# Kernel tuning notes

Hardware: AMD Instinct MI355X
Metric: run time of the kernel (lower is better)

Reference implementation:

```python
import jax, jax.numpy as jnp
import numpy as np

N_NODES = 100000
N_EDGES = 1600000
D_IN = 128
D_EMB = 128


def setup_inputs() -> dict:
    key = jax.random.key(0)
    ks = jax.random.split(key, 8)
    x = jax.random.normal(ks[0], (N_NODES, D_IN), dtype=jnp.float32)
    src = jax.random.randint(ks[1], (N_EDGES,), 0, N_NODES, dtype=jnp.int32)
    dst = jax.random.randint(ks[2], (N_EDGES,), 0, N_NODES, dtype=jnp.int32)
    # Glorot-ish init for GraphConv weights
    s = 1.0 / np.sqrt(D_EMB)
    W0 = jax.random.normal(ks[3], (D_IN, D_EMB), dtype=jnp.float32) * s
    W1 = jax.random.normal(ks[4], (D_EMB, D_EMB), dtype=jnp.float32) * s
    W2 = jax.random.normal(ks[5], (D_EMB, D_EMB), dtype=jnp.float32) * s
    b0 = jnp.zeros((D_EMB,), jnp.float32)
    b1 = jnp.zeros((D_EMB,), jnp.float32)
    b2 = jnp.zeros((D_EMB,), jnp.float32)
    return {"x": x, "src": src, "dst": dst,
            "W0": W0, "b0": b0, "W1": W1, "b1": b1, "W2": W2, "b2": b2}


def _graph_conv(h, src, dst, norm_src, norm_dst, W, b):
    # DGL GraphConv, norm='both': D_out^{-1/2} A D_in^{-1/2} H W + b
    h = h * norm_src[:, None]                       # scale src features
    m = jax.ops.segment_sum(h[src], dst, num_segments=N_NODES)  # SpMM aggregate
    m = m * norm_dst[:, None]
    return m @ W + b


def reference(x, src, dst, W0, b0, W1, b1, W2, b2):
    ones = jnp.ones((N_EDGES,), jnp.float32)
    out_deg = jax.ops.segment_sum(ones, src, num_segments=N_NODES)
    in_deg = jax.ops.segment_sum(ones, dst, num_segments=N_NODES)
    norm_src = jax.lax.rsqrt(jnp.clip(out_deg, 1.0))
    norm_dst = jax.lax.rsqrt(jnp.clip(in_deg, 1.0))

    h = x
    Ws = (W0, W1, W2)
    bs = (b0, b1, b2)
    n_layers = len(Ws)
    for layer in range(n_layers):
        h = _graph_conv(h, src, dst, norm_src, norm_dst, Ws[layer], bs[layer])
        if layer != n_layers - 1:
            h = jax.nn.relu(h)  # dropout is identity in eval mode
    return h
```

## Files before the change

kernel.cpp:

```cpp
#include <hip/hip_runtime.h>
#include <hip/hip_bf16.h>

#define N_NODES 100000
#define N_EDGES 1600000
#define D 128
#define NB 1563
#define PB 256
#define CHUNK 6250
#define SCANL (NB * PB)
#define ECAP 2560

typedef __attribute__((ext_vector_type(8))) short bf16x8;
typedef __attribute__((ext_vector_type(4))) float f32x4;

__device__ __forceinline__ float bf2f(unsigned short u) {
    unsigned int x = ((unsigned int)u) << 16;
    return __builtin_bit_cast(float, x);
}
__device__ __forceinline__ unsigned short f2bf(float f) {
    unsigned int x = __builtin_bit_cast(unsigned int, f);
    x += 0x7fffu + ((x >> 16) & 1u);
    return (unsigned short)(x >> 16);
}

__global__ __launch_bounds__(1024) void k_pcount(const int* __restrict__ src, const int* __restrict__ dst,
                                                 int* __restrict__ cntD, int* __restrict__ cntS) {
    __shared__ int hd[NB];
    __shared__ int hs[NB];
    int t = threadIdx.x, blk = blockIdx.x;
    for (int i = t; i < NB; i += 1024) { hd[i] = 0; hs[i] = 0; }
    __syncthreads();
    int base = blk * CHUNK;
    for (int i = t; i < CHUNK; i += 1024) {
        int e = base + i;
        if (e < N_EDGES) {
            atomicAdd(&hd[dst[e] >> 6], 1);
            atomicAdd(&hs[src[e] >> 6], 1);
        }
    }
    __syncthreads();
    for (int i = t; i < NB; i += 1024) {
        cntD[i * PB + blk] = hd[i];
        cntS[i * PB + blk] = hs[i];
    }
}

__global__ void k_scan1(int* __restrict__ a, int* __restrict__ bs, int n) {
    __shared__ int tmp[256];
    int t = threadIdx.x;
    int i = blockIdx.x * 256 + t;
    int v = (i < n) ? a[i] : 0;
    tmp[t] = v; __syncthreads();
    for (int off = 1; off < 256; off <<= 1) {
        int x = (t >= off) ? tmp[t - off] : 0;
        __syncthreads();
        tmp[t] += x;
        __syncthreads();
    }
    if (i < n) a[i] = tmp[t] - v;
    if (t == 255) bs[blockIdx.x] = tmp[255];
}

__global__ void k_scan2(int* __restrict__ bs, int nb) {
    __shared__ int tmp[1024];
    int t = threadIdx.x;
    int i0 = 2 * t, i1 = 2 * t + 1;
    int a = (i0 < nb) ? bs[i0] : 0;
    int b = (i1 < nb) ? bs[i1] : 0;
    int s = a + b;
    tmp[t] = s; __syncthreads();
    for (int off = 1; off < 1024; off <<= 1) {
        int x = (t >= off) ? tmp[t - off] : 0;
        __syncthreads();
        tmp[t] += x;
        __syncthreads();
    }
    int excl = tmp[t] - s;
    if (i0 < nb) bs[i0] = excl;
    if (i1 < nb) bs[i1] = excl + a;
}

__global__ void k_scan3(int* __restrict__ a, const int* __restrict__ bs, int n) {
    int i = blockIdx.x * 256 + threadIdx.x;
    if (i < n) a[i] += bs[blockIdx.x];
}

__global__ __launch_bounds__(1024) void k_pscatter(const int* __restrict__ src, const int* __restrict__ dst,
                                                   const int* __restrict__ scanD, const int* __restrict__ scanS,
                                                   unsigned int* __restrict__ pairD, unsigned char* __restrict__ srcS) {
    __shared__ int od[NB];
    __shared__ int osx[NB];
    int t = threadIdx.x, blk = blockIdx.x;
    for (int i = t; i < NB; i += 1024) {
        od[i] = scanD[i * PB + blk];
        osx[i] = scanS[i * PB + blk];
    }
    __syncthreads();
    int base = blk * CHUNK;
    for (int i = t; i < CHUNK; i += 1024) {
        int e = base + i;
        if (e < N_EDGES) {
            int s = src[e], d = dst[e];
            int pd = atomicAdd(&od[d >> 6], 1);
            pairD[pd] = ((unsigned int)(d & 63) << 26) | (unsigned int)s;
            int ps = atomicAdd(&osx[s >> 6], 1);
            srcS[ps] = (unsigned char)(s & 63);
        }
    }
}

__global__ __launch_bounds__(256) void k_normsrc(const unsigned char* __restrict__ srcS,
                                                 const int* __restrict__ scanS, float* __restrict__ ns) {
    __shared__ int c[64];
    int b = blockIdx.x, t = threadIdx.x;
    if (t < 64) c[t] = 0;
    __syncthreads();
    int beg = scanS[b * PB];
    int end = (b < NB - 1) ? scanS[(b + 1) * PB] : N_EDGES;
    for (int i = beg + t; i < end; i += 256) atomicAdd(&c[srcS[i]], 1);
    __syncthreads();
    if (t < 64) {
        int g = b * 64 + t;
        if (g < N_NODES) {
            int a = c[t]; if (a < 1) a = 1;
            ns[g] = rsqrtf((float)a);
        }
    }
}

__global__ __launch_bounds__(256) void k_bsort(const unsigned int* __restrict__ pairD,
                                               const int* __restrict__ scanD,
                                               int* __restrict__ esrc,
                                               int* __restrict__ rowbeg,
                                               int* __restrict__ degD) {
    __shared__ int cnt[64], off[64], cur[64];
    int b = blockIdx.x, t = threadIdx.x;
    int lane = t & 63, wave = t >> 6;
    if (t < 64) cnt[t] = 0;
    __syncthreads();
    int beg = scanD[b * PB];
    int end = (b < NB - 1) ? scanD[(b + 1) * PB] : N_EDGES;
    int n = end - beg;
    for (int i = t; i < n; i += 256) atomicAdd(&cnt[pairD[beg + i] >> 26], 1);
    __syncthreads();
    if (wave == 0) {
        int v = cnt[lane];
        int x = v;
        for (int o = 1; o < 64; o <<= 1) { int y = __shfl_up(x, o); if (lane >= o) x += y; }
        off[lane] = x - v;
        cur[lane] = x - v;
    }
    __syncthreads();
    if (t < 64) {
        int g = b * 64 + t;
        if (g < N_NODES) { rowbeg[g] = beg + off[t]; degD[g] = cnt[t]; }
    }
    for (int i = t; i < n; i += 256) {
        unsigned int p = pairD[beg + i];
        int pos = atomicAdd(&cur[p >> 26], 1);
        esrc[beg + pos] = (int)(p & 0x3FFFFFFu);
    }
}

__global__ void k_cvt(const float* __restrict__ x, const float* __restrict__ ns,
                      unsigned short* __restrict__ xb, int n4) {
    int i = blockIdx.x * 256 + threadIdx.x;
    if (i < n4) {
        int row = i >> 5;
        float sc = ns[row];
        const float4 v = ((const float4*)x)[i];
        unsigned int lo = (unsigned int)f2bf(v.x * sc) | ((unsigned int)f2bf(v.y * sc) << 16);
        unsigned int hi = (unsigned int)f2bf(v.z * sc) | ((unsigned int)f2bf(v.w * sc) << 16);
        ((uint2*)xb)[i] = make_uint2(lo, hi);
    }
}

__global__ void k_transw3(const float* __restrict__ W0, const float* __restrict__ W1,
                          const float* __restrict__ W2, unsigned short* __restrict__ Wt) {
    int gid = blockIdx.x * 256 + threadIdx.x;
    if (gid >= 3 * 2048) return;
    int layer = gid >> 11;
    int di8   = gid & 2047;
    const float* W = (layer == 0) ? W0 : ((layer == 1) ? W1 : W2);
    int di   = di8 * 8;
    int lane = di8 & 63;
    int nt   = (di8 >> 6) & 7;
    int kc   = di8 >> 9;
    int quad = lane >> 4, col = lane & 15;
    unsigned short v[8];
#pragma unroll
    for (int j = 0; j < 8; j++) {
        int k = kc * 32 + quad * 8 + j;
        int nn = nt * 16 + col;
        v[j] = f2bf(W[k * 128 + nn]);
    }
    unsigned short* dp = Wt + (size_t)layer * 16384 + di;
#pragma unroll
    for (int j = 0; j < 8; j++) dp[j] = v[j];
}

__device__ __forceinline__ int aswz(int row, int byte16) {
    return row * 256 + (byte16 ^ ((row & 7) << 4));
}

__global__ __launch_bounds__(512) void k_fused(const unsigned short* __restrict__ hin,
        const int* __restrict__ esrc, const int* __restrict__ rowbeg, const int* __restrict__ degD,
        const int* __restrict__ scanD,
        const unsigned short* __restrict__ Wt, const float* __restrict__ bias,
        const float* __restrict__ nsp, unsigned short* __restrict__ Cb, float* __restrict__ Cf, int M) {
    __shared__ int elist[ECAP];
    __shared__ int rb[64], dg[64];
    __shared__ unsigned short lA[64 * 128];
    int b = blockIdx.x, t = threadIdx.x;
    int lane = t & 63, wave = t >> 6;
    int sub = lane >> 4, col = lane & 15;

    int beg = scanD[b * PB];
    int end = (b < NB - 1) ? scanD[(b + 1) * PB] : N_EDGES;
    int cnt = end - beg;
    if (cnt > ECAP) cnt = ECAP;

    if (t < 64) {
        int g = b * 64 + t;
        rb[t] = (g < M) ? rowbeg[g] : beg;
        dg[t] = (g < M) ? degD[g] : 0;
    }
    for (int i = t; i < cnt; i += 512) elist[i] = esrc[beg + i];
    __syncthreads();

    for (int r = wave; r < 64; r += 8) {
        int ro = rb[r] - beg;
        int dgr = dg[r];
        int re = ro + dgr;
        if (re > ECAP) re = ECAP;
        float acc[8];
#pragma unroll
        for (int j = 0; j < 8; j++) acc[j] = 0.f;
        for (int e = ro; e < re; e += 16) {
            int i0 = e + sub, i1 = e + 4 + sub, i2 = e + 8 + sub, i3 = e + 12 + sub;
            bool v0 = i0 < re, v1 = i1 < re, v2 = i2 < re, v3 = i3 < re;
            int s0 = elist[v0 ? i0 : ro];
            int s1 = elist[v1 ? i1 : ro];
            int s2 = elist[v2 ? i2 : ro];
            int s3 = elist[v3 ? i3 : ro];
            uint4 x0 = *(const uint4*)(hin + (size_t)s0 * D + col * 8);
            uint4 x1 = *(const uint4*)(hin + (size_t)s1 * D + col * 8);
            uint4 x2 = *(const uint4*)(hin + (size_t)s2 * D + col * 8);
            uint4 x3 = *(const uint4*)(hin + (size_t)s3 * D + col * 8);
            if (v0) {
                acc[0] += bf2f((unsigned short)x0.x); acc[1] += bf2f((unsigned short)(x0.x >> 16));
                acc[2] += bf2f((unsigned short)x0.y); acc[3] += bf2f((unsigned short)(x0.y >> 16));
                acc[4] += bf2f((unsigned short)x0.z); acc[5] += bf2f((unsigned short)(x0.z >> 16));
                acc[6] += bf2f((unsigned short)x0.w); acc[7] += bf2f((unsigned short)(x0.w >> 16));
            }
            if (v1) {
                acc[0] += bf2f((unsigned short)x1.x); acc[1] += bf2f((unsigned short)(x1.x >> 16));
                acc[2] += bf2f((unsigned short)x1.y); acc[3] += bf2f((unsigned short)(x1.y >> 16));
                acc[4] += bf2f((unsigned short)x1.z); acc[5] += bf2f((unsigned short)(x1.z >> 16));
                acc[6] += bf2f((unsigned short)x1.w); acc[7] += bf2f((unsigned short)(x1.w >> 16));
            }
            if (v2) {
                acc[0] += bf2f((unsigned short)x2.x); acc[1] += bf2f((unsigned short)(x2.x >> 16));
                acc[2] += bf2f((unsigned short)x2.y); acc[3] += bf2f((unsigned short)(x2.y >> 16));
                acc[4] += bf2f((unsigned short)x2.z); acc[5] += bf2f((unsigned short)(x2.z >> 16));
                acc[6] += bf2f((unsigned short)x2.w); acc[7] += bf2f((unsigned short)(x2.w >> 16));
            }
            if (v3) {
                acc[0] += bf2f((unsigned short)x3.x); acc[1] += bf2f((unsigned short)(x3.x >> 16));
                acc[2] += bf2f((unsigned short)x3.y); acc[3] += bf2f((unsigned short)(x3.y >> 16));
                acc[4] += bf2f((unsigned short)x3.z); acc[5] += bf2f((unsigned short)(x3.z >> 16));
                acc[6] += bf2f((unsigned short)x3.w); acc[7] += bf2f((unsigned short)(x3.w >> 16));
            }
        }
#pragma unroll
        for (int j = 0; j < 8; j++) {
            acc[j] += __shfl_xor(acc[j], 16);
            acc[j] += __shfl_xor(acc[j], 32);
        }
        if (sub == 0) {
            int d2 = dgr; if (d2 < 1) d2 = 1;
            float s = rsqrtf((float)d2);
            uint4 o;
            o.x = (unsigned int)f2bf(acc[0] * s) | ((unsigned int)f2bf(acc[1] * s) << 16);
            o.y = (unsigned int)f2bf(acc[2] * s) | ((unsigned int)f2bf(acc[3] * s) << 16);
            o.z = (unsigned int)f2bf(acc[4] * s) | ((unsigned int)f2bf(acc[5] * s) << 16);
            o.w = (unsigned int)f2bf(acc[6] * s) | ((unsigned int)f2bf(acc[7] * s) << 16);
            *(uint4*)((char*)lA + aswz(r, col * 16)) = o;
        }
    }
    __syncthreads();

    int rt = wave & 3;
    int nh = wave >> 2;
    f32x4 acc2[4];
#pragma unroll
    for (int i = 0; i < 4; i++) acc2[i] = (f32x4){0.f, 0.f, 0.f, 0.f};
    int lr = rt * 16 + col;
#pragma unroll
    for (int kc = 0; kc < 4; kc++) {
        bf16x8 af = *(const bf16x8*)((const char*)lA + aswz(lr, kc * 64 + sub * 16));
#pragma unroll
        for (int j = 0; j < 4; j++) {
            int nt = nh * 4 + j;
            bf16x8 bfr = *(const bf16x8*)(Wt + ((size_t)(kc * 8 + nt) * 64 + lane) * 8);
            acc2[j] = __builtin_amdgcn_mfma_f32_16x16x32_bf16(af, bfr, acc2[j], 0, 0, 0);
        }
    }
    int row0 = b * 64 + rt * 16;
#pragma unroll
    for (int j = 0; j < 4; j++) {
        int nt = nh * 4 + j;
        float bv = bias[nt * 16 + col];
#pragma unroll
        for (int r = 0; r < 4; r++) {
            int rr = row0 + sub * 4 + r;
            if (rr < M) {
                float v = acc2[j][r] + bv;
                if (Cf) {
                    Cf[(size_t)rr * D + nt * 16 + col] = v;
                } else {
                    v = fmaxf(v, 0.f) * nsp[rr];
                    Cb[(size_t)rr * D + nt * 16 + col] = f2bf(v);
                }
            }
        }
    }
}

extern "C" void kernel_launch(void* const* d_in, const int* in_sizes, int n_in,
                              void* d_out, int out_size, void* d_ws, size_t ws_size,
                              hipStream_t stream) {
    const float* x  = (const float*)d_in[0];
    const int* src = (const int*)d_in[1];
    const int* dst = (const int*)d_in[2];
    const float* Wl[3] = {(const float*)d_in[3], (const float*)d_in[5], (const float*)d_in[7]};
    const float* Bl[3] = {(const float*)d_in[4], (const float*)d_in[6], (const float*)d_in[8]};

    const int N = N_NODES, E = N_EDGES;
    const int Mpad = ((N + 63) / 64) * 64;

    char* ws = (char*)d_ws;
    size_t o = 0;
    auto take = [&](size_t bytes) -> void* {
        o = (o + 255) & ~(size_t)255;
        void* p = ws + o;
        o += bytes;
        return p;
    };
    int*   cntD     = (int*)take((size_t)SCANL * 4);
    int*   cntS     = (int*)take((size_t)SCANL * 4);
    int*   bsD      = (int*)take(2048 * 4);
    int*   bsS      = (int*)take(2048 * 4);
    float* norm_src = (float*)take((size_t)N * 4);
    unsigned int*  pairD = (unsigned int*)take((size_t)E * 4);
    unsigned char* srcS  = (unsigned char*)take((size_t)E);
    int*   esrc     = (int*)take((size_t)E * 4);
    int*   rowbeg   = (int*)take((size_t)N * 4);
    int*   degD     = (int*)take((size_t)N * 4);
    unsigned short* Wt   = (unsigned short*)take((size_t)3 * 128 * 128 * 2);
    unsigned short* hA   = (unsigned short*)take((size_t)Mpad * D * 2);
    unsigned short* hB   = (unsigned short*)take((size_t)Mpad * D * 2);

    const int sgrid = SCANL / 256;

    k_pcount<<<PB, 1024, 0, stream>>>(src, dst, cntD, cntS);
    k_scan1<<<sgrid, 256, 0, stream>>>(cntD, bsD, SCANL);
    k_scan2<<<1, 1024, 0, stream>>>(bsD, sgrid);
    k_scan3<<<sgrid, 256, 0, stream>>>(cntD, bsD, SCANL);
    k_scan1<<<sgrid, 256, 0, stream>>>(cntS, bsS, SCANL);
    k_scan2<<<1, 1024, 0, stream>>>(bsS, sgrid);
    k_scan3<<<sgrid, 256, 0, stream>>>(cntS, bsS, SCANL);
    k_pscatter<<<PB, 1024, 0, stream>>>(src, dst, cntD, cntS, pairD, srcS);
    k_normsrc<<<NB, 256, 0, stream>>>(srcS, cntS, norm_src);
    k_bsort<<<NB, 256, 0, stream>>>(pairD, cntD, esrc, rowbeg, degD);

    k_cvt<<<(N * 32 + 255) / 256, 256, 0, stream>>>(x, norm_src, hA, N * 32);
    k_transw3<<<24, 256, 0, stream>>>(Wl[0], Wl[1], Wl[2], Wt);

    k_fused<<<NB, 512, 0, stream>>>(hA, esrc, rowbeg, degD, cntD, Wt,           Bl[0], norm_src, hB, nullptr, N);
    k_fused<<<NB, 512, 0, stream>>>(hB, esrc, rowbeg, degD, cntD, Wt + 16384,   Bl[1], norm_src, hA, nullptr, N);
    k_fused<<<NB, 512, 0, stream>>>(hA, esrc, rowbeg, degD, cntD, Wt + 32768,   Bl[2], nullptr,  nullptr, (float*)d_out, N);
}
```

Before: 417.5 us.

## Replace two-level bucket sort with atomic CSR build and padded sentinel rows

Replaces the partitioned count/scan/scatter/bucket-sort pipeline with a direct global-atomic degree count, a single scan over per-node degrees rounded up to multiples of 16, and an atomic scatter into a CSR whose padding slots hold a sentinel index that points at a zeroed row. The aggregation loop can then drop its per-edge validity checks and the LDS edge staging and read esrc directly. The fused kernel also moves to 256 threads with an occupancy hint, and the source norm is recomputed from degrees instead of stored. The trade-offs are global atomic contention in the scatter, roughly doubled edge storage from padding, wasted gathers on padded slots, and edge order within a row that is no longer deterministic.

```diff
diff --git a/kernel.cpp b/kernel.cpp
--- a/kernel.cpp
+++ b/kernel.cpp
@@ -5,10 +5,8 @@
 #define N_EDGES 1600000
 #define D 128
 #define NB 1563
-#define PB 256
-#define CHUNK 6250
-#define SCANL (NB * PB)
-#define ECAP 2560
+#define SENT N_NODES
+#define ECAP_PAD 3200000
 
 typedef __attribute__((ext_vector_type(8))) short bf16x8;
 typedef __attribute__((ext_vector_type(4))) float f32x4;
@@ -23,33 +21,37 @@
     return (unsigned short)(x >> 16);
 }
 
-__global__ __launch_bounds__(1024) void k_pcount(const int* __restrict__ src, const int* __restrict__ dst,
-                                                 int* __restrict__ cntD, int* __restrict__ cntS) {
-    __shared__ int hd[NB];
-    __shared__ int hs[NB];
-    int t = threadIdx.x, blk = blockIdx.x;
-    for (int i = t; i < NB; i += 1024) { hd[i] = 0; hs[i] = 0; }
-    __syncthreads();
-    int base = blk * CHUNK;
-    for (int i = t; i < CHUNK; i += 1024) {
-        int e = base + i;
-        if (e < N_EDGES) {
-            atomicAdd(&hd[dst[e] >> 6], 1);
-            atomicAdd(&hs[src[e] >> 6], 1);
-        }
-    }
-    __syncthreads();
-    for (int i = t; i < NB; i += 1024) {
-        cntD[i * PB + blk] = hd[i];
-        cntS[i * PB + blk] = hs[i];
-    }
-}
-
-__global__ void k_scan1(int* __restrict__ a, int* __restrict__ bs, int n) {
+__global__ __launch_bounds__(256) void k_zero(int* __restrict__ esrc, int* __restrict__ degS,
+                                              int* __restrict__ degD, int* __restrict__ cur,
+                                              unsigned short* __restrict__ hA, unsigned short* __restrict__ hB) {
+    int i = blockIdx.x * 256 + threadIdx.x;
+    if (i < ECAP_PAD / 4) {
+        ((int4*)esrc)[i] = make_int4(SENT, SENT, SENT, SENT);
+    }
+    if (i < N_NODES) { degS[i] = 0; degD[i] = 0; cur[i] = 0; }
+    if (i < 512) {
+        uint4 z = {0u, 0u, 0u, 0u};
+        ((uint4*)(hA + (size_t)N_NODES * D))[i] = z;
+        ((uint4*)(hB + (size_t)N_NODES * D))[i] = z;
+    }
+}
+
+__global__ __launch_bounds__(256) void k_deg(const int* __restrict__ src, const int* __restrict__ dst,
+                                             int* __restrict__ degS, int* __restrict__ degD) {
+    int e = blockIdx.x * 256 + threadIdx.x;
+    if (e < N_EDGES) {
+        atomicAdd(&degS[src[e]], 1);
+        atomicAdd(&degD[dst[e]], 1);
+    }
+}
+
+__global__ void k_scanA(const int* __restrict__ degD, int* __restrict__ rowbeg,
+                        int* __restrict__ bs, int n) {
     __shared__ int tmp[256];
     int t = threadIdx.x;
     int i = blockIdx.x * 256 + t;
-    int v = (i < n) ? a[i] : 0;
+    int v = 0;
+    if (i < n - 1) v = (degD[i] + 15) & ~15;
     tmp[t] = v; __syncthreads();
     for (int off = 1; off < 256; off <<= 1) {
         int x = (t >= off) ? tmp[t - off] : 0;
@@ -57,7 +59,7 @@
         tmp[t] += x;
         __syncthreads();
     }
-    if (i < n) a[i] = tmp[t] - v;
+    if (i < n) rowbeg[i] = tmp[t] - v;
     if (t == 255) bs[blockIdx.x] = tmp[255];
 }
 
@@ -85,89 +87,24 @@
     if (i < n) a[i] += bs[blockIdx.x];
 }
 
-__global__ __launch_bounds__(1024) void k_pscatter(const int* __restrict__ src, const int* __restrict__ dst,
-                                                   const int* __restrict__ scanD, const int* __restrict__ scanS,
-                                                   unsigned int* __restrict__ pairD, unsigned char* __restrict__ srcS) {
-    __shared__ int od[NB];
-    __shared__ int osx[NB];
-    int t = threadIdx.x, blk = blockIdx.x;
-    for (int i = t; i < NB; i += 1024) {
-        od[i] = scanD[i * PB + blk];
-        osx[i] = scanS[i * PB + blk];
-    }
-    __syncthreads();
-    int base = blk * CHUNK;
-    for (int i = t; i < CHUNK; i += 1024) {
-        int e = base + i;
-        if (e < N_EDGES) {
-            int s = src[e], d = dst[e];
-            int pd = atomicAdd(&od[d >> 6], 1);
-            pairD[pd] = ((unsigned int)(d & 63) << 26) | (unsigned int)s;
-            int ps = atomicAdd(&osx[s >> 6], 1);
-            srcS[ps] = (unsigned char)(s & 63);
-        }
-    }
-}
-
-__global__ __launch_bounds__(256) void k_normsrc(const unsigned char* __restrict__ srcS,
-                                                 const int* __restrict__ scanS, float* __restrict__ ns) {
-    __shared__ int c[64];
-    int b = blockIdx.x, t = threadIdx.x;
-    if (t < 64) c[t] = 0;
-    __syncthreads();
-    int beg = scanS[b * PB];
-    int end = (b < NB - 1) ? scanS[(b + 1) * PB] : N_EDGES;
-    for (int i = beg + t; i < end; i += 256) atomicAdd(&c[srcS[i]], 1);
-    __syncthreads();
-    if (t < 64) {
-        int g = b * 64 + t;
-        if (g < N_NODES) {
-            int a = c[t]; if (a < 1) a = 1;
-            ns[g] = rsqrtf((float)a);
-        }
-    }
-}
-
-__global__ __launch_bounds__(256) void k_bsort(const unsigned int* __restrict__ pairD,
-                                               const int* __restrict__ scanD,
-                                               int* __restrict__ esrc,
-                                               int* __restrict__ rowbeg,
-                                               int* __restrict__ degD) {
-    __shared__ int cnt[64], off[64], cur[64];
-    int b = blockIdx.x, t = threadIdx.x;
-    int lane = t & 63, wave = t >> 6;
-    if (t < 64) cnt[t] = 0;
-    __syncthreads();
-    int beg = scanD[b * PB];
-    int end = (b < NB - 1) ? scanD[(b + 1) * PB] : N_EDGES;
-    int n = end - beg;
-    for (int i = t; i < n; i += 256) atomicAdd(&cnt[pairD[beg + i] >> 26], 1);
-    __syncthreads();
-    if (wave == 0) {
-        int v = cnt[lane];
-        int x = v;
-        for (int o = 1; o < 64; o <<= 1) { int y = __shfl_up(x, o); if (lane >= o) x += y; }
-        off[lane] = x - v;
-        cur[lane] = x - v;
-    }
-    __syncthreads();
-    if (t < 64) {
-        int g = b * 64 + t;
-        if (g < N_NODES) { rowbeg[g] = beg + off[t]; degD[g] = cnt[t]; }
-    }
-    for (int i = t; i < n; i += 256) {
-        unsigned int p = pairD[beg + i];
-        int pos = atomicAdd(&cur[p >> 26], 1);
-        esrc[beg + pos] = (int)(p & 0x3FFFFFFu);
-    }
-}
-
-__global__ void k_cvt(const float* __restrict__ x, const float* __restrict__ ns,
+__global__ __launch_bounds__(256) void k_scatter(const int* __restrict__ src, const int* __restrict__ dst,
+                                                 const int* __restrict__ rowbeg, int* __restrict__ cur,
+                                                 int* __restrict__ esrc) {
+    int e = blockIdx.x * 256 + threadIdx.x;
+    if (e < N_EDGES) {
+        int d = dst[e];
+        int pos = atomicAdd(&cur[d], 1);
+        esrc[rowbeg[d] + pos] = src[e];
+    }
+}
+
+__global__ void k_cvt(const float* __restrict__ x, const int* __restrict__ degS,
                       unsigned short* __restrict__ xb, int n4) {
     int i = blockIdx.x * 256 + threadIdx.x;
     if (i < n4) {
         int row = i >> 5;
-        float sc = ns[row];
+        int dg = degS[row]; if (dg < 1) dg = 1;
+        float sc = rsqrtf((float)dg);
         const float4 v = ((const float4*)x)[i];
         unsigned int lo = (unsigned int)f2bf(v.x * sc) | ((unsigned int)f2bf(v.y * sc) << 16);
         unsigned int hi = (unsigned int)f2bf(v.z * sc) | ((unsigned int)f2bf(v.w * sc) << 16);
@@ -203,74 +140,60 @@
     return row * 256 + (byte16 ^ ((row & 7) << 4));
 }
 
-__global__ __launch_bounds__(512) void k_fused(const unsigned short* __restrict__ hin,
+__global__ __launch_bounds__(256, 8) void k_fused(const unsigned short* __restrict__ hin,
         const int* __restrict__ esrc, const int* __restrict__ rowbeg, const int* __restrict__ degD,
-        const int* __restrict__ scanD,
+        const int* __restrict__ degS,
         const unsigned short* __restrict__ Wt, const float* __restrict__ bias,
-        const float* __restrict__ nsp, unsigned short* __restrict__ Cb, float* __restrict__ Cf, int M) {
-    __shared__ int elist[ECAP];
-    __shared__ int rb[64], dg[64];
+        unsigned short* __restrict__ Cb, float* __restrict__ Cf, int M) {
+    __shared__ int rb[65];
+    __shared__ int dgt[64];
     __shared__ unsigned short lA[64 * 128];
     int b = blockIdx.x, t = threadIdx.x;
     int lane = t & 63, wave = t >> 6;
     int sub = lane >> 4, col = lane & 15;
 
-    int beg = scanD[b * PB];
-    int end = (b < NB - 1) ? scanD[(b + 1) * PB] : N_EDGES;
-    int cnt = end - beg;
-    if (cnt > ECAP) cnt = ECAP;
-
-    if (t < 64) {
+    if (t < 65) {
         int g = b * 64 + t;
-        rb[t] = (g < M) ? rowbeg[g] : beg;
-        dg[t] = (g < M) ? degD[g] : 0;
-    }
-    for (int i = t; i < cnt; i += 512) elist[i] = esrc[beg + i];
+        if (g > N_NODES) g = N_NODES;
+        rb[t] = rowbeg[g];
+        if (t < 64) {
+            int g2 = b * 64 + t;
+            dgt[t] = (g2 < M) ? degD[g2] : 0;
+        }
+    }
     __syncthreads();
 
-    for (int r = wave; r < 64; r += 8) {
-        int ro = rb[r] - beg;
-        int dgr = dg[r];
-        int re = ro + dgr;
-        if (re > ECAP) re = ECAP;
+    for (int r = wave; r < 64; r += 4) {
+        int ro = rb[r];
+        int re = rb[r + 1];
         float acc[8];
 #pragma unroll
         for (int j = 0; j < 8; j++) acc[j] = 0.f;
         for (int e = ro; e < re; e += 16) {
-            int i0 = e + sub, i1 = e + 4 + sub, i2 = e + 8 + sub, i3 = e + 12 + sub;
-            bool v0 = i0 < re, v1 = i1 < re, v2 = i2 < re, v3 = i3 < re;
-            int s0 = elist[v0 ? i0 : ro];
-            int s1 = elist[v1 ? i1 : ro];
-            int s2 = elist[v2 ? i2 : ro];
-            int s3 = elist[v3 ? i3 : ro];
+            int s0 = esrc[e + sub];
+            int s1 = esrc[e + 4 + sub];
+            int s2 = esrc[e + 8 + sub];
+            int s3 = esrc[e + 12 + sub];
             uint4 x0 = *(const uint4*)(hin + (size_t)s0 * D + col * 8);
             uint4 x1 = *(const uint4*)(hin + (size_t)s1 * D + col * 8);
             uint4 x2 = *(const uint4*)(hin + (size_t)s2 * D + col * 8);
             uint4 x3 = *(const uint4*)(hin + (size_t)s3 * D + col * 8);
-            if (v0) {
-                acc[0] += bf2f((unsigned short)x0.x); acc[1] += bf2f((unsigned short)(x0.x >> 16));
-                acc[2] += bf2f((unsigned short)x0.y); acc[3] += bf2f((unsigned short)(x0.y >> 16));
-                acc[4] += bf2f((unsigned short)x0.z); acc[5] += bf2f((unsigned short)(x0.z >> 16));
-                acc[6] += bf2f((unsigned short)x0.w); acc[7] += bf2f((unsigned short)(x0.w >> 16));
-            }
-            if (v1) {
-                acc[0] += bf2f((unsigned short)x1.x); acc[1] += bf2f((unsigned short)(x1.x >> 16));
-                acc[2] += bf2f((unsigned short)x1.y); acc[3] += bf2f((unsigned short)(x1.y >> 16));
-                acc[4] += bf2f((unsigned short)x1.z); acc[5] += bf2f((unsigned short)(x1.z >> 16));
-                acc[6] += bf2f((unsigned short)x1.w); acc[7] += bf2f((unsigned short)(x1.w >> 16));
-            }
-            if (v2) {
-                acc[0] += bf2f((unsigned short)x2.x); acc[1] += bf2f((unsigned short)(x2.x >> 16));
-                acc[2] += bf2f((unsigned short)x2.y); acc[3] += bf2f((unsigned short)(x2.y >> 16));
-                acc[4] += bf2f((unsigned short)x2.z); acc[5] += bf2f((unsigned short)(x2.z >> 16));
-                acc[6] += bf2f((unsigned short)x2.w); acc[7] += bf2f((unsigned short)(x2.w >> 16));
-            }
-            if (v3) {
-                acc[0] += bf2f((unsigned short)x3.x); acc[1] += bf2f((unsigned short)(x3.x >> 16));
-                acc[2] += bf2f((unsigned short)x3.y); acc[3] += bf2f((unsigned short)(x3.y >> 16));
-                acc[4] += bf2f((unsigned short)x3.z); acc[5] += bf2f((unsigned short)(x3.z >> 16));
-                acc[6] += bf2f((unsigned short)x3.w); acc[7] += bf2f((unsigned short)(x3.w >> 16));
-            }
+            acc[0] += bf2f((unsigned short)x0.x); acc[1] += bf2f((unsigned short)(x0.x >> 16));
+            acc[2] += bf2f((unsigned short)x0.y); acc[3] += bf2f((unsigned short)(x0.y >> 16));
+            acc[4] += bf2f((unsigned short)x0.z); acc[5] += bf2f((unsigned short)(x0.z >> 16));
+            acc[6] += bf2f((unsigned short)x0.w); acc[7] += bf2f((unsigned short)(x0.w >> 16));
+            acc[0] += bf2f((unsigned short)x1.x); acc[1] += bf2f((unsigned short)(x1.x >> 16));
+            acc[2] += bf2f((unsigned short)x1.y); acc[3] += bf2f((unsigned short)(x1.y >> 16));
+            acc[4] += bf2f((unsigned short)x1.z); acc[5] += bf2f((unsigned short)(x1.z >> 16));
+            acc[6] += bf2f((unsigned short)x1.w); acc[7] += bf2f((unsigned short)(x1.w >> 16));
+            acc[0] += bf2f((unsigned short)x2.x); acc[1] += bf2f((unsigned short)(x2.x >> 16));
+            acc[2] += bf2f((unsigned short)x2.y); acc[3] += bf2f((unsigned short)(x2.y >> 16));
+            acc[4] += bf2f((unsigned short)x2.z); acc[5] += bf2f((unsigned short)(x2.z >> 16));
+            acc[6] += bf2f((unsigned short)x2.w); acc[7] += bf2f((unsigned short)(x2.w >> 16));
+            acc[0] += bf2f((unsigned short)x3.x); acc[1] += bf2f((unsigned short)(x3.x >> 16));
+            acc[2] += bf2f((unsigned short)x3.y); acc[3] += bf2f((unsigned short)(x3.y >> 16));
+            acc[4] += bf2f((unsigned short)x3.z); acc[5] += bf2f((unsigned short)(x3.z >> 16));
+            acc[6] += bf2f((unsigned short)x3.w); acc[7] += bf2f((unsigned short)(x3.w >> 16));
         }
 #pragma unroll
         for (int j = 0; j < 8; j++) {
@@ -278,7 +201,7 @@
             acc[j] += __shfl_xor(acc[j], 32);
         }
         if (sub == 0) {
-            int d2 = dgr; if (d2 < 1) d2 = 1;
+            int d2 = dgt[r]; if (d2 < 1) d2 = 1;
             float s = rsqrtf((float)d2);
             uint4 o;
             o.x = (unsigned int)f2bf(acc[0] * s) | ((unsigned int)f2bf(acc[1] * s) << 16);
@@ -290,37 +213,48 @@
     }
     __syncthreads();
 
-    int rt = wave & 3;
-    int nh = wave >> 2;
-    f32x4 acc2[4];
-#pragma unroll
-    for (int i = 0; i < 4; i++) acc2[i] = (f32x4){0.f, 0.f, 0.f, 0.f};
-    int lr = rt * 16 + col;
-#pragma unroll
-    for (int kc = 0; kc < 4; kc++) {
-        bf16x8 af = *(const bf16x8*)((const char*)lA + aswz(lr, kc * 64 + sub * 16));
-#pragma unroll
-        for (int j = 0; j < 4; j++) {
-            int nt = nh * 4 + j;
-            bf16x8 bfr = *(const bf16x8*)(Wt + ((size_t)(kc * 8 + nt) * 64 + lane) * 8);
-            acc2[j] = __builtin_amdgcn_mfma_f32_16x16x32_bf16(af, bfr, acc2[j], 0, 0, 0);
-        }
-    }
-    int row0 = b * 64 + rt * 16;
-#pragma unroll
-    for (int j = 0; j < 4; j++) {
-        int nt = nh * 4 + j;
-        float bv = bias[nt * 16 + col];
+    int row0 = b * 64 + wave * 16;
+    float nsv[4];
+    if (Cb) {
 #pragma unroll
         for (int r = 0; r < 4; r++) {
             int rr = row0 + sub * 4 + r;
-            if (rr < M) {
-                float v = acc2[j][r] + bv;
-                if (Cf) {
-                    Cf[(size_t)rr * D + nt * 16 + col] = v;
-                } else {
-                    v = fmaxf(v, 0.f) * nsp[rr];
-                    Cb[(size_t)rr * D + nt * 16 + col] = f2bf(v);
+            int dg = (rr < M) ? degS[rr] : 1;
+            if (dg < 1) dg = 1;
+            nsv[r] = rsqrtf((float)dg);
+        }
+    }
+#pragma unroll
+    for (int half = 0; half < 2; half++) {
+        f32x4 acc2[4];
+#pragma unroll
+        for (int i = 0; i < 4; i++) acc2[i] = (f32x4){0.f, 0.f, 0.f, 0.f};
+        int lr = wave * 16 + col;
+#pragma unroll
+        for (int kc = 0; kc < 4; kc++) {
+            bf16x8 af = *(const bf16x8*)((const char*)lA + aswz(lr, kc * 64 + sub * 16));
+#pragma unroll
+            for (int j = 0; j < 4; j++) {
+                int nt = half * 4 + j;
+                bf16x8 bfr = *(const bf16x8*)(Wt + ((size_t)(kc * 8 + nt) * 64 + lane) * 8);
+                acc2[j] = __builtin_amdgcn_mfma_f32_16x16x32_bf16(af, bfr, acc2[j], 0, 0, 0);
+            }
+        }
+#pragma unroll
+        for (int j = 0; j < 4; j++) {
+            int nt = half * 4 + j;
+            float bv = bias[nt * 16 + col];
+#pragma unroll
+            for (int r = 0; r < 4; r++) {
+                int rr = row0 + sub * 4 + r;
+                if (rr < M) {
+                    float v = acc2[j][r] + bv;
+                    if (Cf) {
+                        Cf[(size_t)rr * D + nt * 16 + col] = v;
+                    } else {
+                        v = fmaxf(v, 0.f) * nsv[r];
+                        Cb[(size_t)rr * D + nt * 16 + col] = f2bf(v);
+                    }
                 }
             }
         }
@@ -347,37 +281,29 @@
         o += bytes;
         return p;
     };
-    int*   cntD     = (int*)take((size_t)SCANL * 4);
-    int*   cntS     = (int*)take((size_t)SCANL * 4);
-    int*   bsD      = (int*)take(2048 * 4);
-    int*   bsS      = (int*)take(2048 * 4);
-    float* norm_src = (float*)take((size_t)N * 4);
-    unsigned int*  pairD = (unsigned int*)take((size_t)E * 4);
-    unsigned char* srcS  = (unsigned char*)take((size_t)E);
-    int*   esrc     = (int*)take((size_t)E * 4);
-    int*   rowbeg   = (int*)take((size_t)N * 4);
+    int*   degS     = (int*)take((size_t)N * 4);
     int*   degD     = (int*)take((size_t)N * 4);
+    int*   cur      = (int*)take((size_t)N * 4);
+    int*   rowbeg   = (int*)take((size_t)(N + 1) * 4);
+    int*   bsc      = (int*)take(2048 * 4);
+    int*   esrc     = (int*)take((size_t)ECAP_PAD * 4);
     unsigned short* Wt   = (unsigned short*)take((size_t)3 * 128 * 128 * 2);
     unsigned short* hA   = (unsigned short*)take((size_t)Mpad * D * 2);
     unsigned short* hB   = (unsigned short*)take((size_t)Mpad * D * 2);
 
-    const int sgrid = SCANL / 256;
-
-    k_pcount<<<PB, 1024, 0, stream>>>(src, dst, cntD, cntS);
-    k_scan1<<<sgrid, 256, 0, stream>>>(cntD, bsD, SCANL);
-    k_scan2<<<1, 1024, 0, stream>>>(bsD, sgrid);
-    k_scan3<<<sgrid, 256, 0, stream>>>(cntD, bsD, SCANL);
-    k_scan1<<<sgrid, 256, 0, stream>>>(cntS, bsS, SCANL);
-    k_scan2<<<1, 1024, 0, stream>>>(bsS, sgrid);
-    k_scan3<<<sgrid, 256, 0, stream>>>(cntS, bsS, SCANL);
-    k_pscatter<<<PB, 1024, 0, stream>>>(src, dst, cntD, cntS, pairD, srcS);
-    k_normsrc<<<NB, 256, 0, stream>>>(srcS, cntS, norm_src);
-    k_bsort<<<NB, 256, 0, stream>>>(pairD, cntD, esrc, rowbeg, degD);
-
-    k_cvt<<<(N * 32 + 255) / 256, 256, 0, stream>>>(x, norm_src, hA, N * 32);
+    const int scangrid = (N + 1 + 255) / 256;
+
+    k_zero<<<(ECAP_PAD / 4 + 255) / 256, 256, 0, stream>>>(esrc, degS, degD, cur, hA, hB);
+    k_deg<<<(E + 255) / 256, 256, 0, stream>>>(src, dst, degS, degD);
+    k_scanA<<<scangrid, 256, 0, stream>>>(degD, rowbeg, bsc, N + 1);
+    k_scan2<<<1, 1024, 0, stream>>>(bsc, scangrid);
+    k_scan3<<<scangrid, 256, 0, stream>>>(rowbeg, bsc, N + 1);
+    k_scatter<<<(E + 255) / 256, 256, 0, stream>>>(src, dst, rowbeg, cur, esrc);
+
+    k_cvt<<<(N * 32 + 255) / 256, 256, 0, stream>>>(x, degS, hA, N * 32);
     k_transw3<<<24, 256, 0, stream>>>(Wl[0], Wl[1], Wl[2], Wt);
 
-    k_fused<<<NB, 512, 0, stream>>>(hA, esrc, rowbeg, degD, cntD, Wt,           Bl[0], norm_src, hB, nullptr, N);
-    k_fused<<<NB, 512, 0, stream>>>(hB, esrc, rowbeg, degD, cntD, Wt + 16384,   Bl[1], norm_src, hA, nullptr, N);
-    k_fused<<<NB, 512, 0, stream>>>(hA, esrc, rowbeg, degD, cntD, Wt + 32768,   Bl[2], nullptr,  nullptr, (float*)d_out, N);
-}
+    k_fused<<<NB, 256, 0, stream>>>(hA, esrc, rowbeg, degD, degS, Wt,         Bl[0], hB, nullptr, N);
+    k_fused<<<NB, 256, 0, stream>>>(hB, esrc, rowbeg, degD, degS, Wt + 16384, Bl[1], hA, nullptr, N);
+    k_fused<<<NB, 256, 0, stream>>>(hA, esrc, rowbeg, degD, degS, Wt + 32768, Bl[2], nullptr, (float*)d_out, N);
+}
```

After: 542.5 us. 1.3x slower.

## Pad CSR rows to multiples of four with sentinel, drop LDS edge staging

Applied to the files above, without the earlier changes.

Each destination row's edge list is padded to a multiple of 4 with a sentinel index that points at a zeroed feature row, so the gather loop needs no per-edge validity masks. The fused kernel now reads edge indices straight from global memory instead of staging them in LDS. It also drops to 256 threads per block with higher occupancy, each wave computing both column halves of the MFMA epilogue. Separately, the D/S scans are merged into fewer launches and redundant bounds checks are removed. Padding adds some wasted gathers of the zero row and grows the edge buffer.

```diff
diff --git a/kernel.cpp b/kernel.cpp
--- a/kernel.cpp
+++ b/kernel.cpp
@@ -8,7 +8,9 @@
 #define PB 256
 #define CHUNK 6250
 #define SCANL (NB * PB)
-#define ECAP 2560
+#define SGRID (SCANL / 256)
+#define SENT N_NODES
+#define ECAP_PAD (N_EDGES + 256 * NB)
 
 typedef __attribute__((ext_vector_type(8))) short bf16x8;
 typedef __attribute__((ext_vector_type(4))) float f32x4;
@@ -21,6 +23,12 @@
     unsigned int x = __builtin_bit_cast(unsigned int, f);
     x += 0x7fffu + ((x >> 16) & 1u);
     return (unsigned short)(x >> 16);
+}
+__device__ __forceinline__ void accum8(float* acc, uint4 x) {
+    acc[0] += bf2f((unsigned short)x.x); acc[1] += bf2f((unsigned short)(x.x >> 16));
+    acc[2] += bf2f((unsigned short)x.y); acc[3] += bf2f((unsigned short)(x.y >> 16));
+    acc[4] += bf2f((unsigned short)x.z); acc[5] += bf2f((unsigned short)(x.z >> 16));
+    acc[6] += bf2f((unsigned short)x.w); acc[7] += bf2f((unsigned short)(x.w >> 16));
 }
 
 __global__ __launch_bounds__(1024) void k_pcount(const int* __restrict__ src, const int* __restrict__ dst,
@@ -33,10 +41,8 @@
     int base = blk * CHUNK;
     for (int i = t; i < CHUNK; i += 1024) {
         int e = base + i;
-        if (e < N_EDGES) {
-            atomicAdd(&hd[dst[e] >> 6], 1);
-            atomicAdd(&hs[src[e] >> 6], 1);
-        }
+        atomicAdd(&hd[dst[e] >> 6], 1);
+        atomicAdd(&hs[src[e] >> 6], 1);
     }
     __syncthreads();
     for (int i = t; i < NB; i += 1024) {
@@ -45,11 +51,14 @@
     }
 }
 
-__global__ void k_scan1(int* __restrict__ a, int* __restrict__ bs, int n) {
+__global__ void k_scanDS1(int* __restrict__ cntD, int* __restrict__ cntS, int* __restrict__ bs) {
     __shared__ int tmp[256];
     int t = threadIdx.x;
-    int i = blockIdx.x * 256 + t;
-    int v = (i < n) ? a[i] : 0;
+    int which = (blockIdx.x >= SGRID) ? 1 : 0;
+    int blk = blockIdx.x - which * SGRID;
+    int* a = which ? cntS : cntD;
+    int i = blk * 256 + t;
+    int v = a[i];
     tmp[t] = v; __syncthreads();
     for (int off = 1; off < 256; off <<= 1) {
         int x = (t >= off) ? tmp[t - off] : 0;
@@ -57,16 +66,17 @@
         tmp[t] += x;
         __syncthreads();
     }
-    if (i < n) a[i] = tmp[t] - v;
+    a[i] = tmp[t] - v;
     if (t == 255) bs[blockIdx.x] = tmp[255];
 }
 
-__global__ void k_scan2(int* __restrict__ bs, int nb) {
+__global__ void k_scan2two(int* __restrict__ bs) {
     __shared__ int tmp[1024];
     int t = threadIdx.x;
+    int base = blockIdx.x * SGRID;
     int i0 = 2 * t, i1 = 2 * t + 1;
-    int a = (i0 < nb) ? bs[i0] : 0;
-    int b = (i1 < nb) ? bs[i1] : 0;
+    int a = (i0 < SGRID) ? bs[base + i0] : 0;
+    int b = (i1 < SGRID) ? bs[base + i1] : 0;
     int s = a + b;
     tmp[t] = s; __syncthreads();
     for (int off = 1; off < 1024; off <<= 1) {
@@ -76,13 +86,15 @@
         __syncthreads();
     }
     int excl = tmp[t] - s;
-    if (i0 < nb) bs[i0] = excl;
-    if (i1 < nb) bs[i1] = excl + a;
-}
-
-__global__ void k_scan3(int* __restrict__ a, const int* __restrict__ bs, int n) {
-    int i = blockIdx.x * 256 + threadIdx.x;
-    if (i < n) a[i] += bs[blockIdx.x];
+    if (i0 < SGRID) bs[base + i0] = excl;
+    if (i1 < SGRID) bs[base + i1] = excl + a;
+}
+
+__global__ void k_scanDS3(int* __restrict__ cntD, int* __restrict__ cntS, const int* __restrict__ bs) {
+    int which = (blockIdx.x >= SGRID) ? 1 : 0;
+    int blk = blockIdx.x - which * SGRID;
+    int* a = which ? cntS : cntD;
+    a[blk * 256 + threadIdx.x] += bs[blockIdx.x];
 }
 
 __global__ __launch_bounds__(1024) void k_pscatter(const int* __restrict__ src, const int* __restrict__ dst,
@@ -99,13 +111,11 @@
     int base = blk * CHUNK;
     for (int i = t; i < CHUNK; i += 1024) {
         int e = base + i;
-        if (e < N_EDGES) {
-            int s = src[e], d = dst[e];
-            int pd = atomicAdd(&od[d >> 6], 1);
-            pairD[pd] = ((unsigned int)(d & 63) << 26) | (unsigned int)s;
-            int ps = atomicAdd(&osx[s >> 6], 1);
-            srcS[ps] = (unsigned char)(s & 63);
-        }
+        int s = src[e], d = dst[e];
+        int pd = atomicAdd(&od[d >> 6], 1);
+        pairD[pd] = ((unsigned int)(d & 63) << 26) | (unsigned int)s;
+        int ps = atomicAdd(&osx[s >> 6], 1);
+        srcS[ps] = (unsigned char)(s & 63);
     }
 }
 
@@ -128,11 +138,11 @@
     }
 }
 
-__global__ __launch_bounds__(256) void k_bsort(const unsigned int* __restrict__ pairD,
-                                               const int* __restrict__ scanD,
-                                               int* __restrict__ esrc,
-                                               int* __restrict__ rowbeg,
-                                               int* __restrict__ degD) {
+__global__ __launch_bounds__(256) void k_bsortpad(const unsigned int* __restrict__ pairD,
+                                                  const int* __restrict__ scanD,
+                                                  int* __restrict__ esrc,
+                                                  int* __restrict__ rowbeg,
+                                                  int* __restrict__ degD) {
     __shared__ int cnt[64], off[64], cur[64];
     int b = blockIdx.x, t = threadIdx.x;
     int lane = t & 63, wave = t >> 6;
@@ -141,29 +151,37 @@
     int beg = scanD[b * PB];
     int end = (b < NB - 1) ? scanD[(b + 1) * PB] : N_EDGES;
     int n = end - beg;
+    int base = beg + 256 * b;
     for (int i = t; i < n; i += 256) atomicAdd(&cnt[pairD[beg + i] >> 26], 1);
     __syncthreads();
     if (wave == 0) {
         int v = cnt[lane];
-        int x = v;
+        int pc = (v + 3) & ~3;
+        int x = pc;
         for (int o = 1; o < 64; o <<= 1) { int y = __shfl_up(x, o); if (lane >= o) x += y; }
-        off[lane] = x - v;
-        cur[lane] = x - v;
+        off[lane] = x - pc;
+        cur[lane] = x - pc;
     }
     __syncthreads();
     if (t < 64) {
         int g = b * 64 + t;
-        if (g < N_NODES) { rowbeg[g] = beg + off[t]; degD[g] = cnt[t]; }
+        if (g < N_NODES) { rowbeg[g] = base + off[t]; degD[g] = cnt[t]; }
+    }
+    {
+        int r = t >> 2, j = t & 3;
+        int c0 = cnt[r];
+        int slot = off[r] + c0 + j;
+        if (slot < off[r] + ((c0 + 3) & ~3)) esrc[base + slot] = SENT;
     }
     for (int i = t; i < n; i += 256) {
         unsigned int p = pairD[beg + i];
         int pos = atomicAdd(&cur[p >> 26], 1);
-        esrc[beg + pos] = (int)(p & 0x3FFFFFFu);
+        esrc[base + pos] = (int)(p & 0x3FFFFFFu);
     }
 }
 
 __global__ void k_cvt(const float* __restrict__ x, const float* __restrict__ ns,
-                      unsigned short* __restrict__ xb, int n4) {
+                      unsigned short* __restrict__ hA, unsigned short* __restrict__ hB, int n4) {
     int i = blockIdx.x * 256 + threadIdx.x;
     if (i < n4) {
         int row = i >> 5;
@@ -171,7 +189,12 @@
         const float4 v = ((const float4*)x)[i];
         unsigned int lo = (unsigned int)f2bf(v.x * sc) | ((unsigned int)f2bf(v.y * sc) << 16);
         unsigned int hi = (unsigned int)f2bf(v.z * sc) | ((unsigned int)f2bf(v.w * sc) << 16);
-        ((uint2*)xb)[i] = make_uint2(lo, hi);
+        ((uint2*)hA)[i] = make_uint2(lo, hi);
+    } else if (i < n4 + 64) {
+        int j = i - n4;
+        uint2 z = {0u, 0u};
+        if (j < 32) ((uint2*)(hA + (size_t)SENT * D))[j] = z;
+        else        ((uint2*)(hB + (size_t)SENT * D))[j - 32] = z;
     }
 }
 
@@ -203,74 +226,48 @@
     return row * 256 + (byte16 ^ ((row & 7) << 4));
 }
 
-__global__ __launch_bounds__(512) void k_fused(const unsigned short* __restrict__ hin,
+__global__ __launch_bounds__(256, 8) void k_fused(const unsigned short* __restrict__ hin,
         const int* __restrict__ esrc, const int* __restrict__ rowbeg, const int* __restrict__ degD,
-        const int* __restrict__ scanD,
+        const float* __restrict__ nsp,
         const unsigned short* __restrict__ Wt, const float* __restrict__ bias,
-        const float* __restrict__ nsp, unsigned short* __restrict__ Cb, float* __restrict__ Cf, int M) {
-    __shared__ int elist[ECAP];
-    __shared__ int rb[64], dg[64];
+        unsigned short* __restrict__ Cb, float* __restrict__ Cf, int M) {
+    __shared__ int rb[64];
+    __shared__ int dgt[64];
     __shared__ unsigned short lA[64 * 128];
     int b = blockIdx.x, t = threadIdx.x;
     int lane = t & 63, wave = t >> 6;
     int sub = lane >> 4, col = lane & 15;
 
-    int beg = scanD[b * PB];
-    int end = (b < NB - 1) ? scanD[(b + 1) * PB] : N_EDGES;
-    int cnt = end - beg;
-    if (cnt > ECAP) cnt = ECAP;
-
     if (t < 64) {
         int g = b * 64 + t;
-        rb[t] = (g < M) ? rowbeg[g] : beg;
-        dg[t] = (g < M) ? degD[g] : 0;
-    }
-    for (int i = t; i < cnt; i += 512) elist[i] = esrc[beg + i];
-    __syncthreads();
-
-    for (int r = wave; r < 64; r += 8) {
-        int ro = rb[r] - beg;
-        int dgr = dg[r];
-        int re = ro + dgr;
-        if (re > ECAP) re = ECAP;
+        rb[t]  = (g < M) ? rowbeg[g] : 0;
+        dgt[t] = (g < M) ? degD[g] : 0;
+    }
+    __syncthreads();
+
+    for (int r = wave; r < 64; r += 4) {
+        int ro = rb[r];
+        int dgr = dgt[r];
+        int re = ro + ((dgr + 3) & ~3);
         float acc[8];
 #pragma unroll
         for (int j = 0; j < 8; j++) acc[j] = 0.f;
-        for (int e = ro; e < re; e += 16) {
-            int i0 = e + sub, i1 = e + 4 + sub, i2 = e + 8 + sub, i3 = e + 12 + sub;
-            bool v0 = i0 < re, v1 = i1 < re, v2 = i2 < re, v3 = i3 < re;
-            int s0 = elist[v0 ? i0 : ro];
-            int s1 = elist[v1 ? i1 : ro];
-            int s2 = elist[v2 ? i2 : ro];
-            int s3 = elist[v3 ? i3 : ro];
+        int e = ro;
+        for (; e + 16 <= re; e += 16) {
+            int s0 = esrc[e + sub];
+            int s1 = esrc[e + 4 + sub];
+            int s2 = esrc[e + 8 + sub];
+            int s3 = esrc[e + 12 + sub];
             uint4 x0 = *(const uint4*)(hin + (size_t)s0 * D + col * 8);
             uint4 x1 = *(const uint4*)(hin + (size_t)s1 * D + col * 8);
             uint4 x2 = *(const uint4*)(hin + (size_t)s2 * D + col * 8);
             uint4 x3 = *(const uint4*)(hin + (size_t)s3 * D + col * 8);
-            if (v0) {
-                acc[0] += bf2f((unsigned short)x0.x); acc[1] += bf2f((unsigned short)(x0.x >> 16));
-                acc[2] += bf2f((unsigned short)x0.y); acc[3] += bf2f((unsigned short)(x0.y >> 16));
-                acc[4] += bf2f((unsigned short)x0.z); acc[5] += bf2f((unsigned short)(x0.z >> 16));
-                acc[6] += bf2f((unsigned short)x0.w); acc[7] += bf2f((unsigned short)(x0.w >> 16));
-            }
-            if (v1) {
-                acc[0] += bf2f((unsigned short)x1.x); acc[1] += bf2f((unsigned short)(x1.x >> 16));
-                acc[2] += bf2f((unsigned short)x1.y); acc[3] += bf2f((unsigned short)(x1.y >> 16));
-                acc[4] += bf2f((unsigned short)x1.z); acc[5] += bf2f((unsigned short)(x1.z >> 16));
-                acc[6] += bf2f((unsigned short)x1.w); acc[7] += bf2f((unsigned short)(x1.w >> 16));
-            }
-            if (v2) {
-                acc[0] += bf2f((unsigned short)x2.x); acc[1] += bf2f((unsigned short)(x2.x >> 16));
-                acc[2] += bf2f((unsigned short)x2.y); acc[3] += bf2f((unsigned short)(x2.y >> 16));
-                acc[4] += bf2f((unsigned short)x2.z); acc[5] += bf2f((unsigned short)(x2.z >> 16));
-                acc[6] += bf2f((unsigned short)x2.w); acc[7] += bf2f((unsigned short)(x2.w >> 16));
-            }
-            if (v3) {
-                acc[0] += bf2f((unsigned short)x3.x); acc[1] += bf2f((unsigned short)(x3.x >> 16));
-                acc[2] += bf2f((unsigned short)x3.y); acc[3] += bf2f((unsigned short)(x3.y >> 16));
-                acc[4] += bf2f((unsigned short)x3.z); acc[5] += bf2f((unsigned short)(x3.z >> 16));
-                acc[6] += bf2f((unsigned short)x3.w); acc[7] += bf2f((unsigned short)(x3.w >> 16));
-            }
+            accum8(acc, x0); accum8(acc, x1); accum8(acc, x2); accum8(acc, x3);
+        }
+        for (; e < re; e += 4) {
+            int s = esrc[e + sub];
+            uint4 x = *(const uint4*)(hin + (size_t)s * D + col * 8);
+            accum8(acc, x);
         }
 #pragma unroll
         for (int j = 0; j < 8; j++) {
@@ -290,37 +287,46 @@
     }
     __syncthreads();
 
-    int rt = wave & 3;
-    int nh = wave >> 2;
-    f32x4 acc2[4];
-#pragma unroll
-    for (int i = 0; i < 4; i++) acc2[i] = (f32x4){0.f, 0.f, 0.f, 0.f};
-    int lr = rt * 16 + col;
-#pragma unroll
-    for (int kc = 0; kc < 4; kc++) {
-        bf16x8 af = *(const bf16x8*)((const char*)lA + aswz(lr, kc * 64 + sub * 16));
-#pragma unroll
-        for (int j = 0; j < 4; j++) {
-            int nt = nh * 4 + j;
-            bf16x8 bfr = *(const bf16x8*)(Wt + ((size_t)(kc * 8 + nt) * 64 + lane) * 8);
-            acc2[j] = __builtin_amdgcn_mfma_f32_16x16x32_bf16(af, bfr, acc2[j], 0, 0, 0);
-        }
-    }
-    int row0 = b * 64 + rt * 16;
-#pragma unroll
-    for (int j = 0; j < 4; j++) {
-        int nt = nh * 4 + j;
-        float bv = bias[nt * 16 + col];
+    int row0 = b * 64 + wave * 16;
+    float nsv[4];
+    if (Cb) {
 #pragma unroll
         for (int r = 0; r < 4; r++) {
             int rr = row0 + sub * 4 + r;
-            if (rr < M) {
-                float v = acc2[j][r] + bv;
-                if (Cf) {
-                    Cf[(size_t)rr * D + nt * 16 + col] = v;
-                } else {
-                    v = fmaxf(v, 0.f) * nsp[rr];
-                    Cb[(size_t)rr * D + nt * 16 + col] = f2bf(v);
+            nsv[r] = (rr < M) ? nsp[rr] : 1.f;
+        }
+    }
+#pragma unroll
+    for (int half = 0; half < 2; half++) {
+        f32x4 acc2[4];
+#pragma unroll
+        for (int i = 0; i < 4; i++) acc2[i] = (f32x4){0.f, 0.f, 0.f, 0.f};
+        int lr = wave * 16 + col;
+#pragma unroll
+        for (int kc = 0; kc < 4; kc++) {
+            bf16x8 af = *(const bf16x8*)((const char*)lA + aswz(lr, kc * 64 + sub * 16));
+#pragma unroll
+            for (int j = 0; j < 4; j++) {
+                int nt = half * 4 + j;
+                bf16x8 bfr = *(const bf16x8*)(Wt + ((size_t)(kc * 8 + nt) * 64 + lane) * 8);
+                acc2[j] = __builtin_amdgcn_mfma_f32_16x16x32_bf16(af, bfr, acc2[j], 0, 0, 0);
+            }
+        }
+#pragma unroll
+        for (int j = 0; j < 4; j++) {
+            int nt = half * 4 + j;
+            float bv = bias[nt * 16 + col];
+#pragma unroll
+            for (int r = 0; r < 4; r++) {
+                int rr = row0 + sub * 4 + r;
+                if (rr < M) {
+                    float v = acc2[j][r] + bv;
+                    if (Cf) {
+                        Cf[(size_t)rr * D + nt * 16 + col] = v;
+                    } else {
+                        v = fmaxf(v, 0.f) * nsv[r];
+                        Cb[(size_t)rr * D + nt * 16 + col] = f2bf(v);
+                    }
                 }
             }
         }
@@ -336,7 +342,7 @@
     const float* Wl[3] = {(const float*)d_in[3], (const float*)d_in[5], (const float*)d_in[7]};
     const float* Bl[3] = {(const float*)d_in[4], (const float*)d_in[6], (const float*)d_in[8]};
 
-    const int N = N_NODES, E = N_EDGES;
+    const int N = N_NODES;
     const int Mpad = ((N + 63) / 64) * 64;
 
     char* ws = (char*)d_ws;
@@ -349,35 +355,29 @@
     };
     int*   cntD     = (int*)take((size_t)SCANL * 4);
     int*   cntS     = (int*)take((size_t)SCANL * 4);
-    int*   bsD      = (int*)take(2048 * 4);
-    int*   bsS      = (int*)take(2048 * 4);
+    int*   bs       = (int*)take((size_t)2 * SGRID * 4);
     float* norm_src = (float*)take((size_t)N * 4);
-    unsigned int*  pairD = (unsigned int*)take((size_t)E * 4);
-    unsigned char* srcS  = (unsigned char*)take((size_t)E);
-    int*   esrc     = (int*)take((size_t)E * 4);
+    unsigned int*  pairD = (unsigned int*)take((size_t)N_EDGES * 4);
+    unsigned char* srcS  = (unsigned char*)take((size_t)N_EDGES);
+    int*   esrc     = (int*)take((size_t)ECAP_PAD * 4);
     int*   rowbeg   = (int*)take((size_t)N * 4);
     int*   degD     = (int*)take((size_t)N * 4);
     unsigned short* Wt   = (unsigned short*)take((size_t)3 * 128 * 128 * 2);
     unsigned short* hA   = (unsigned short*)take((size_t)Mpad * D * 2);
     unsigned short* hB   = (unsigned short*)take((size_t)Mpad * D * 2);
 
-    const int sgrid = SCANL / 256;
-
     k_pcount<<<PB, 1024, 0, stream>>>(src, dst, cntD, cntS);
-    k_scan1<<<sgrid, 256, 0, stream>>>(cntD, bsD, SCANL);
-    k_scan2<<<1, 1024, 0, stream>>>(bsD, sgrid);
-    k_scan3<<<sgrid, 256, 0, stream>>>(cntD, bsD, SCANL);
-    k_scan1<<<sgrid, 256, 0, stream>>>(cntS, bsS, SCANL);
-    k_scan2<<<1, 1024, 0, stream>>>(bsS, sgrid);
-    k_scan3<<<sgrid, 256, 0, stream>>>(cntS, bsS, SCANL);
+    k_scanDS1<<<2 * SGRID, 256, 0, stream>>>(cntD, cntS, bs);
+    k_scan2two<<<2, 1024, 0, stream>>>(bs);
+    k_scanDS3<<<2 * SGRID, 256, 0, stream>>>(cntD, cntS, bs);
     k_pscatter<<<PB, 1024, 0, stream>>>(src, dst, cntD, cntS, pairD, srcS);
     k_normsrc<<<NB, 256, 0, stream>>>(srcS, cntS, norm_src);
-    k_bsort<<<NB, 256, 0, stream>>>(pairD, cntD, esrc, rowbeg, degD);
-
-    k_cvt<<<(N * 32 + 255) / 256, 256, 0, stream>>>(x, norm_src, hA, N * 32);
+    k_bsortpad<<<NB, 256, 0, stream>>>(pairD, cntD, esrc, rowbeg, degD);
+
+    k_cvt<<<(N * 32 + 64 + 255) / 256, 256, 0, stream>>>(x, norm_src, hA, hB, N * 32);
     k_transw3<<<24, 256, 0, stream>>>(Wl[0], Wl[1], Wl[2], Wt);
 
-    k_fused<<<NB, 512, 0, stream>>>(hA, esrc, rowbeg, degD, cntD, Wt,           Bl[0], norm_src, hB, nullptr, N);
-    k_fused<<<NB, 512, 0, stream>>>(hB, esrc, rowbeg, degD, cntD, Wt + 16384,   Bl[1], norm_src, hA, nullptr, N);
-    k_fused<<<NB, 512, 0, stream>>>(hA, esrc, rowbeg, degD, cntD, Wt + 32768,   Bl[2], nullptr,  nullptr, (float*)d_out, N);
-}
+    k_fused<<<NB, 256, 0, stream>>>(hA, esrc, rowbeg, degD, norm_src, Wt,         Bl[0], hB, nullptr, N);
+    k_fused<<<NB, 256, 0, stream>>>(hB, esrc, rowbeg, degD, norm_src, Wt + 16384, Bl[1], hA, nullptr, N);
+    k_fused<<<NB, 256, 0, stream>>>(hA, esrc, rowbeg, degD, norm_src, Wt + 32768, Bl[2], nullptr, (float*)d_out, N);
+}
```

New measurement: 408.4 us. -2.2%, faster.
